# Performance work log

Measured on AMD Instinct MI355X. Metric: run time of the kernel, lower is better.

The kernel has to match this reference:

```python
import jax, jax.numpy as jnp
import numpy as np


def setup_inputs() -> dict:
    key = jax.random.key(0)
    ks = jax.random.split(key, 9)
    N, C, H, W, K = 8, 512, 64, 64, 32
    C4 = C // 4
    s = lambda k, shape, scale=0.02: jax.random.normal(k, shape, dtype=jnp.float32) * scale
    return {
        "x": jax.random.normal(ks[0], (N, C, H, W), dtype=jnp.float32),
        "y": jax.random.normal(ks[1], (N, K, C), dtype=jnp.float32),
        "wq": s(ks[2], (C4, C)),
        "bq": s(ks[3], (C4,)),
        "wk": s(ks[4], (C4, C)),
        "bk": s(ks[5], (C4,)),
        "wv": s(ks[6], (C, C)),
        "bv": s(ks[7], (C,)),
        "scale": s(ks[8], (1,), 1.0),
    }


def reference(x, y, wq, bq, wk, bk, wv, bv, scale):
    N, C, H, W = x.shape
    # 1x1 conv query: (N,C,H,W) -> (N,C4,H,W) -> (N, HW, C4)
    q = jnp.einsum('nchw,oc->nhwo', x, wq) + bq  # (N,H,W,C4)
    q = q.reshape(N, H * W, -1)                   # (N, HW, C4)
    # key/value linears on centers y: (N,K,C)
    k = y @ wk.T + bk                             # (N, K, C4)
    v = y @ wv.T + bv                             # (N, K, C)
    energy = jnp.einsum('npc,nkc->npk', q, k)     # (N, HW, K)
    attn = jax.nn.softmax(energy, axis=-1)
    out = jnp.einsum('nkc,npk->ncp', v, attn)     # (N, C, HW)
    out = out.reshape(N, C, H, W)
    return scale[0] * out + x
```

## Files before the change

### kernel.cpp

```cpp
#include <hip/hip_runtime.h>


#define N_  8
#define C_  512
#define HW_ 4096
#define K_  32

typedef __attribute__((ext_vector_type(8))) short bf16x8;
typedef __attribute__((ext_vector_type(4))) float f32x4;
typedef __attribute__((ext_vector_type(4))) unsigned short u16x4;
typedef __attribute__((ext_vector_type(4))) int i32x4;

__device__ __forceinline__ unsigned short f2b(float f) {
    union { float f; unsigned u; } v; v.f = f;
    unsigned r = v.u + 0x7FFFu + ((v.u >> 16) & 1u);
    return (unsigned short)(r >> 16);
}
__device__ __forceinline__ float b2f(unsigned short h) {
    union { unsigned u; float f; } v; v.u = ((unsigned)h) << 16; return v.f;
}
__device__ __forceinline__ int cvtpk(float a, float b) {
    int r;
    asm("v_cvt_pk_bf16_f32 %0, %1, %2" : "=v"(r) : "v"(a), "v"(b));
    return r;
}

__device__ __forceinline__ int wqk_idx(int kk, int c) {
    return ((((c >> 5) * 2 + (kk >> 4)) * 64 + ((c >> 3) & 3) * 16 + (kk & 15)) << 3) + (c & 7);
}

__global__ __launch_bounds__(256) void prep_kernel(
    const float* __restrict__ y, const float* __restrict__ wq, const float* __restrict__ bq,
    const float* __restrict__ wk, const float* __restrict__ bk,
    const float* __restrict__ wv, const float* __restrict__ bv,
    unsigned short* __restrict__ wqkf, float* __restrict__ bqk, unsigned short* __restrict__ vtf)
{
    const int bid = blockIdx.x;
    const int t = threadIdx.x;

    if (bid < 256) {
        __shared__ float vred[3][4][16][8];
        const int n   = bid >> 5;
        const int ct  = bid & 31;
        const int cl  = t & 15;
        const int kko = (t >> 4) & 3;
        const int jq4 = t >> 6;
        const int c   = ct * 16 + cl;

        const float* yb  = y  + ((size_t)n * K_ + kko * 8) * C_ + jq4 * 128;
        const float* wvb = wv + (size_t)c * C_ + jq4 * 128;
        float acc[8] = {0,0,0,0,0,0,0,0};
        #pragma unroll 4
        for (int jj = 0; jj < 32; ++jj) {
            float4 w4 = *(const float4*)(wvb + jj * 4);
            #pragma unroll
            for (int u = 0; u < 8; ++u) {
                float4 y4 = *(const float4*)(yb + (size_t)u * C_ + jj * 4);
                acc[u] += y4.x * w4.x + y4.y * w4.y + y4.z * w4.z + y4.w * w4.w;
            }
        }
        if (jq4 > 0) {
            #pragma unroll
            for (int u = 0; u < 8; ++u) vred[jq4 - 1][kko][cl][u] = acc[u];
        }
        __syncthreads();
        if (jq4 == 0) {
            const float bvc = bv[c];
            unsigned short o[8];
            #pragma unroll
            for (int u = 0; u < 8; ++u) {
                float s = acc[u] + vred[0][kko][cl][u] + vred[1][kko][cl][u]
                        + vred[2][kko][cl][u] + bvc;
                o[u] = f2b(s);
            }
            i32x4 pk = { (int)(o[0] | ((unsigned)o[1] << 16)), (int)(o[2] | ((unsigned)o[3] << 16)),
                         (int)(o[4] | ((unsigned)o[5] << 16)), (int)(o[6] | ((unsigned)o[7] << 16)) };
            *(i32x4*)(vtf + (size_t)n * (K_ * C_) + (size_t)((ct * 64 + kko * 16 + cl) * 8)) = pk;
        }
    } else {
        __shared__ __align__(16) float kp[2][128];
        __shared__ __align__(16) float kr[128];
        const int b = bid - 256;
        const int n = b >> 5, kk = b & 31;
        const int o = t & 127, half = t >> 7;

        const float* yb  = y  + ((size_t)n * K_ + kk) * C_ + half * 256;
        const float* wkb = wk + (size_t)o * C_ + half * 256;
        float a = 0.f;
        #pragma unroll 4
        for (int jq = 0; jq < 64; ++jq) {
            float4 w4 = *(const float4*)(wkb + jq * 4);
            float4 y4 = *(const float4*)(yb + jq * 4);
            a += y4.x * w4.x + y4.y * w4.y + y4.z * w4.z + y4.w * w4.w;
        }
        kp[half][o] = a;
        __syncthreads();
        if (t < 128) kr[t] = kp[0][t] + kp[1][t] + bk[t];
        __syncthreads();
        if (t < 64) {
            float s = kr[t] * bq[t] + kr[t + 64] * bq[t + 64];
            #pragma unroll
            for (int d = 32; d > 0; d >>= 1) s += __shfl_down(s, d);
            if (t == 0) bqk[n * K_ + kk] = s;
        }
        const int c1 = t, c2 = t + 256;
        float s1 = 0.f, s2 = 0.f;
        for (int oq = 0; oq < 32; ++oq) {
            float4 k4 = *(const float4*)(&kr[oq * 4]);
            const float* wq0 = wq + (size_t)(oq * 4) * C_;
            s1 += k4.x * wq0[c1] + k4.y * wq0[C_ + c1] + k4.z * wq0[2*C_ + c1] + k4.w * wq0[3*C_ + c1];
            s2 += k4.x * wq0[c2] + k4.y * wq0[C_ + c2] + k4.z * wq0[2*C_ + c2] + k4.w * wq0[3*C_ + c2];
        }
        unsigned short* wqf_n = wqkf + (size_t)n * (K_ * C_);
        wqf_n[wqk_idx(kk, c1)] = f2b(s1);
        wqf_n[wqk_idx(kk, c2)] = f2b(s2);
    }
}

__global__ __launch_bounds__(256) void main_kernel(
    const float* __restrict__ x, const unsigned short* __restrict__ wqkf,
    const unsigned short* __restrict__ vtf, const float* __restrict__ bqk,
    const float* __restrict__ scale, float* __restrict__ out)
{
    __shared__ __align__(16) unsigned short xl[16384];
    __shared__ float e_lds[32][36];

    const int bid = (blockIdx.x & 7) * 128 + (blockIdx.x >> 3);
    const int n  = bid >> 7;
    const int p0 = (bid & 127) * 32;
    const int t  = threadIdx.x;
    const int w  = t >> 6, l = t & 63;
    const int l15 = l & 15, lg = l >> 4;
    const float* xg = x + (size_t)n * C_ * HW_;
    float* og = out + (size_t)n * C_ * HW_;
    const unsigned short* wqf  = wqkf + (size_t)n * (K_ * C_);
    const unsigned short* vtfn = vtf  + (size_t)n * (K_ * C_);

    const int mh = w;
    const int kt = w >> 1;
    bf16x8 vf[8];
    #pragma unroll
    for (int mi = 0; mi < 8; ++mi)
        vf[mi] = *(const bf16x8*)(vtfn + ((size_t)(mh * 8 + mi) * 64 + l) * 8);
    bf16x8 b0 = *(const bf16x8*)(wqf + ((size_t)(0 * 2 + kt) * 64 + l) * 8);
    bf16x8 b1 = *(const bf16x8*)(wqf + ((size_t)(1 * 2 + kt) * 64 + l) * 8);

    const int px = t & 31, g = t >> 5;
    const float* xc = xg + p0 + px;
    const int pt = w & 1;
    f32x4 acc = {0.f, 0.f, 0.f, 0.f};
    const unsigned short* xbase = xl + lg * 256 + (pt * 16 + l15) * 8;

    {
        float r0[4][8];
        #pragma unroll
        for (int u = 0; u < 4; ++u)
            #pragma unroll
            for (int j = 0; j < 8; ++j)
                r0[u][j] = xc[(size_t)(g * 8 + u * 64 + j) * HW_];
        #pragma unroll
        for (int u = 0; u < 4; ++u) {
            const int cbase = g * 8 + u * 64;
            const int elem = ((cbase >> 5) * 1024) + (((cbase >> 3) & 3) * 256) + px * 8;
            i32x4 pk = { cvtpk(r0[u][0], r0[u][1]), cvtpk(r0[u][2], r0[u][3]),
                         cvtpk(r0[u][4], r0[u][5]), cvtpk(r0[u][6], r0[u][7]) };
            *(i32x4*)(xl + elem) = pk;
        }
    }
    __syncthreads();

    {
        float r1[4][8];
        #pragma unroll
        for (int u = 0; u < 4; ++u)
            #pragma unroll
            for (int j = 0; j < 8; ++j)
                r1[u][j] = xc[(size_t)(g * 8 + (u + 4) * 64 + j) * HW_];

        for (int cs = 0; cs < 8; ++cs) {
            bf16x8 b2 = *(const bf16x8*)(wqf + ((size_t)((cs + 2) * 2 + kt) * 64 + l) * 8);
            const bf16x8 af = *(const bf16x8*)(xbase + cs * 1024);
            acc = __builtin_amdgcn_mfma_f32_16x16x32_bf16(af, b0, acc, 0, 0, 0);
            b0 = b1; b1 = b2;
        }

        #pragma unroll
        for (int u = 0; u < 4; ++u) {
            const int cbase = g * 8 + (u + 4) * 64;
            const int elem = ((cbase >> 5) * 1024) + (((cbase >> 3) & 3) * 256) + px * 8;
            i32x4 pk = { cvtpk(r1[u][0], r1[u][1]), cvtpk(r1[u][2], r1[u][3]),
                         cvtpk(r1[u][4], r1[u][5]), cvtpk(r1[u][6], r1[u][7]) };
            *(i32x4*)(xl + elem) = pk;
        }
    }
    __syncthreads();

    {
        for (int cs = 8; cs < 16; ++cs) {
            bf16x8 b2;
            if (cs < 14) b2 = *(const bf16x8*)(wqf + ((size_t)((cs + 2) * 2 + kt) * 64 + l) * 8);
            const bf16x8 af = *(const bf16x8*)(xbase + cs * 1024);
            acc = __builtin_amdgcn_mfma_f32_16x16x32_bf16(af, b0, acc, 0, 0, 0);
            b0 = b1; b1 = b2;
        }
        const float bq_ = bqk[n * K_ + kt * 16 + l15];
        #pragma unroll
        for (int r = 0; r < 4; ++r)
            e_lds[pt * 16 + lg * 4 + r][kt * 16 + l15] = acc[r] + bq_;
    }
    __syncthreads();

    bf16x8 paf0, paf1;
    {
        float e0[32], e1[32];
        #pragma unroll
        for (int i = 0; i < 8; ++i) {
            float4 q0 = *(const float4*)&e_lds[l15][4 * i];
            float4 q1 = *(const float4*)&e_lds[16 + l15][4 * i];
            e0[4*i] = q0.x; e0[4*i+1] = q0.y; e0[4*i+2] = q0.z; e0[4*i+3] = q0.w;
            e1[4*i] = q1.x; e1[4*i+1] = q1.y; e1[4*i+2] = q1.z; e1[4*i+3] = q1.w;
        }
        float m0 = e0[0], m1 = e1[0];
        #pragma unroll
        for (int k = 1; k < 32; ++k) { m0 = fmaxf(m0, e0[k]); m1 = fmaxf(m1, e1[k]); }
        float s0 = 0.f, s1 = 0.f;
        #pragma unroll
        for (int k = 0; k < 32; ++k) {
            e0[k] = __expf(e0[k] - m0); s0 += e0[k];
            e1[k] = __expf(e1[k] - m1); s1 += e1[k];
        }
        const float i0 = 1.f / s0, i1 = 1.f / s1;
        union { int i[4]; bf16x8 v; } u0, u1;
        #pragma unroll
        for (int jj = 0; jj < 4; ++jj) {
            u0.i[jj] = cvtpk(e0[8*lg + 2*jj] * i0, e0[8*lg + 2*jj + 1] * i0);
            u1.i[jj] = cvtpk(e1[8*lg + 2*jj] * i1, e1[8*lg + 2*jj + 1] * i1);
        }
        paf0 = u0.v; paf1 = u1.v;
    }

    {
        const float fs = scale[0];
        const int pxa = p0 + l15, pxb = p0 + 16 + l15;
        const int mt0 = mh * 8;

        #pragma unroll
        for (int mi = 0; mi < 8; ++mi) {
            const int mt = mt0 + mi;
            f32x4 d0 = __builtin_amdgcn_mfma_f32_16x16x32_bf16(vf[mi], paf0, (f32x4){0.f,0.f,0.f,0.f}, 0, 0, 0);
            f32x4 d1 = __builtin_amdgcn_mfma_f32_16x16x32_bf16(vf[mi], paf1, (f32x4){0.f,0.f,0.f,0.f}, 0, 0, 0);
            const int base = (mt >> 1) * 1024 + ((2 * mt + (lg >> 1)) & 3) * 256 + (lg & 1) * 4;
            const u16x4 ra = *(const u16x4*)(xl + base + l15 * 8);
            const u16x4 rb = *(const u16x4*)(xl + base + (16 + l15) * 8);
            const int cc = mt * 16 + lg * 4;
            #pragma unroll
            for (int r = 0; r < 4; ++r) {
                og[(size_t)(cc + r) * HW_ + pxa] = fs * d0[r] + b2f(ra[r]);
                og[(size_t)(cc + r) * HW_ + pxb] = fs * d1[r] + b2f(rb[r]);
            }
        }
    }
}

extern "C" void kernel_launch(void* const* d_in, const int* in_sizes, int n_in,
                              void* d_out, int out_size, void* d_ws, size_t ws_size,
                              hipStream_t stream) {
    const float* x     = (const float*)d_in[0];
    const float* y     = (const float*)d_in[1];
    const float* wq    = (const float*)d_in[2];
    const float* bq    = (const float*)d_in[3];
    const float* wk    = (const float*)d_in[4];
    const float* bk    = (const float*)d_in[5];
    const float* wv    = (const float*)d_in[6];
    const float* bv    = (const float*)d_in[7];
    const float* scale = (const float*)d_in[8];

    unsigned short* wqkf = (unsigned short*)d_ws;
    unsigned short* vtf  = wqkf + (size_t)N_ * K_ * C_;
    float* bqk = (float*)((char*)d_ws + 524288);

    prep_kernel<<<512, 256, 0, stream>>>(y, wq, bq, wk, bk, wv, bv, wqkf, bqk, vtf);
    main_kernel<<<1024, 256, 0, stream>>>(x, wqkf, vtf, bqk, scale, (float*)d_out);
}
```

Measured before the change: 54.70 us.

## Process two pixel tiles per block with double-buffered LDS prefetch

Each block now handles two consecutive 32-pixel tiles, and the grid is halved to 512 blocks. The x slab for the second tile is loaded from global memory into registers and written into a second LDS buffer while the first tile's energy, softmax and output stages run. The V fragments, bias and scale are loaded once and reused for both tiles. The cost is double the LDS footprint (64KB for x), which reduces occupancy, and fewer blocks in flight. Overlap within a block also shrinks, because the first tile's x load is no longer split around the first half of the QK MFMAs.

```diff
diff --git a/kernel.cpp b/kernel.cpp
--- a/kernel.cpp
+++ b/kernel.cpp
@@ -122,12 +122,12 @@
     const unsigned short* __restrict__ vtf, const float* __restrict__ bqk,
     const float* __restrict__ scale, float* __restrict__ out)
 {
-    __shared__ __align__(16) unsigned short xl[16384];
+    __shared__ __align__(16) unsigned short xl[2][16384];
     __shared__ float e_lds[32][36];
 
-    const int bid = (blockIdx.x & 7) * 128 + (blockIdx.x >> 3);
-    const int n  = bid >> 7;
-    const int p0 = (bid & 127) * 32;
+    const int swz = (blockIdx.x & 7) * 64 + (blockIdx.x >> 3);
+    const int n    = swz >> 6;
+    const int pair = swz & 63;
     const int t  = threadIdx.x;
     const int w  = t >> 6, l = t & 63;
     const int l15 = l & 15, lg = l >> 4;
@@ -138,127 +138,147 @@
 
     const int mh = w;
     const int kt = w >> 1;
+    const int pt = w & 1;
+    const int px = t & 31, g = t >> 5;
+    const float fs = scale[0];
+    const float bq_ = bqk[n * K_ + kt * 16 + l15];
+
     bf16x8 vf[8];
     #pragma unroll
     for (int mi = 0; mi < 8; ++mi)
         vf[mi] = *(const bf16x8*)(vtfn + ((size_t)(mh * 8 + mi) * 64 + l) * 8);
-    bf16x8 b0 = *(const bf16x8*)(wqf + ((size_t)(0 * 2 + kt) * 64 + l) * 8);
-    bf16x8 b1 = *(const bf16x8*)(wqf + ((size_t)(1 * 2 + kt) * 64 + l) * 8);
-
-    const int px = t & 31, g = t >> 5;
-    const float* xc = xg + p0 + px;
-    const int pt = w & 1;
-    f32x4 acc = {0.f, 0.f, 0.f, 0.f};
-    const unsigned short* xbase = xl + lg * 256 + (pt * 16 + l15) * 8;
 
     {
-        float r0[4][8];
+        const float* xc = xg + pair * 64 + px;
+        float r[4][8];
         #pragma unroll
-        for (int u = 0; u < 4; ++u)
-            #pragma unroll
-            for (int j = 0; j < 8; ++j)
-                r0[u][j] = xc[(size_t)(g * 8 + u * 64 + j) * HW_];
-        #pragma unroll
-        for (int u = 0; u < 4; ++u) {
-            const int cbase = g * 8 + u * 64;
-            const int elem = ((cbase >> 5) * 1024) + (((cbase >> 3) & 3) * 256) + px * 8;
-            i32x4 pk = { cvtpk(r0[u][0], r0[u][1]), cvtpk(r0[u][2], r0[u][3]),
-                         cvtpk(r0[u][4], r0[u][5]), cvtpk(r0[u][6], r0[u][7]) };
-            *(i32x4*)(xl + elem) = pk;
+        for (int h = 0; h < 2; ++h) {
+            #pragma unroll
+            for (int u = 0; u < 4; ++u)
+                #pragma unroll
+                for (int j = 0; j < 8; ++j)
+                    r[u][j] = xc[(size_t)(g * 8 + (h * 4 + u) * 64 + j) * HW_];
+            #pragma unroll
+            for (int u = 0; u < 4; ++u) {
+                const int cbase = g * 8 + (h * 4 + u) * 64;
+                const int elem = ((cbase >> 5) * 1024) + (((cbase >> 3) & 3) * 256) + px * 8;
+                i32x4 pk = { cvtpk(r[u][0], r[u][1]), cvtpk(r[u][2], r[u][3]),
+                             cvtpk(r[u][4], r[u][5]), cvtpk(r[u][6], r[u][7]) };
+                *(i32x4*)(&xl[0][elem]) = pk;
+            }
         }
     }
     __syncthreads();
 
-    {
-        float r1[4][8];
-        #pragma unroll
-        for (int u = 0; u < 4; ++u)
-            #pragma unroll
-            for (int j = 0; j < 8; ++j)
-                r1[u][j] = xc[(size_t)(g * 8 + (u + 4) * 64 + j) * HW_];
-
-        for (int cs = 0; cs < 8; ++cs) {
-            bf16x8 b2 = *(const bf16x8*)(wqf + ((size_t)((cs + 2) * 2 + kt) * 64 + l) * 8);
-            const bf16x8 af = *(const bf16x8*)(xbase + cs * 1024);
-            acc = __builtin_amdgcn_mfma_f32_16x16x32_bf16(af, b0, acc, 0, 0, 0);
-            b0 = b1; b1 = b2;
-        }
-
-        #pragma unroll
-        for (int u = 0; u < 4; ++u) {
-            const int cbase = g * 8 + (u + 4) * 64;
-            const int elem = ((cbase >> 5) * 1024) + (((cbase >> 3) & 3) * 256) + px * 8;
-            i32x4 pk = { cvtpk(r1[u][0], r1[u][1]), cvtpk(r1[u][2], r1[u][3]),
-                         cvtpk(r1[u][4], r1[u][5]), cvtpk(r1[u][6], r1[u][7]) };
-            *(i32x4*)(xl + elem) = pk;
-        }
-    }
-    __syncthreads();
-
-    {
-        for (int cs = 8; cs < 16; ++cs) {
-            bf16x8 b2;
-            if (cs < 14) b2 = *(const bf16x8*)(wqf + ((size_t)((cs + 2) * 2 + kt) * 64 + l) * 8);
-            const bf16x8 af = *(const bf16x8*)(xbase + cs * 1024);
-            acc = __builtin_amdgcn_mfma_f32_16x16x32_bf16(af, b0, acc, 0, 0, 0);
-            b0 = b1; b1 = b2;
-        }
-        const float bq_ = bqk[n * K_ + kt * 16 + l15];
-        #pragma unroll
-        for (int r = 0; r < 4; ++r)
-            e_lds[pt * 16 + lg * 4 + r][kt * 16 + l15] = acc[r] + bq_;
-    }
-    __syncthreads();
-
-    bf16x8 paf0, paf1;
-    {
-        float e0[32], e1[32];
-        #pragma unroll
-        for (int i = 0; i < 8; ++i) {
-            float4 q0 = *(const float4*)&e_lds[l15][4 * i];
-            float4 q1 = *(const float4*)&e_lds[16 + l15][4 * i];
-            e0[4*i] = q0.x; e0[4*i+1] = q0.y; e0[4*i+2] = q0.z; e0[4*i+3] = q0.w;
-            e1[4*i] = q1.x; e1[4*i+1] = q1.y; e1[4*i+2] = q1.z; e1[4*i+3] = q1.w;
-        }
-        float m0 = e0[0], m1 = e1[0];
-        #pragma unroll
-        for (int k = 1; k < 32; ++k) { m0 = fmaxf(m0, e0[k]); m1 = fmaxf(m1, e1[k]); }
-        float s0 = 0.f, s1 = 0.f;
-        #pragma unroll
-        for (int k = 0; k < 32; ++k) {
-            e0[k] = __expf(e0[k] - m0); s0 += e0[k];
-            e1[k] = __expf(e1[k] - m1); s1 += e1[k];
-        }
-        const float i0 = 1.f / s0, i1 = 1.f / s1;
-        union { int i[4]; bf16x8 v; } u0, u1;
-        #pragma unroll
-        for (int jj = 0; jj < 4; ++jj) {
-            u0.i[jj] = cvtpk(e0[8*lg + 2*jj] * i0, e0[8*lg + 2*jj + 1] * i0);
-            u1.i[jj] = cvtpk(e1[8*lg + 2*jj] * i1, e1[8*lg + 2*jj + 1] * i1);
-        }
-        paf0 = u0.v; paf1 = u1.v;
-    }
-
-    {
-        const float fs = scale[0];
-        const int pxa = p0 + l15, pxb = p0 + 16 + l15;
-        const int mt0 = mh * 8;
-
-        #pragma unroll
-        for (int mi = 0; mi < 8; ++mi) {
-            const int mt = mt0 + mi;
-            f32x4 d0 = __builtin_amdgcn_mfma_f32_16x16x32_bf16(vf[mi], paf0, (f32x4){0.f,0.f,0.f,0.f}, 0, 0, 0);
-            f32x4 d1 = __builtin_amdgcn_mfma_f32_16x16x32_bf16(vf[mi], paf1, (f32x4){0.f,0.f,0.f,0.f}, 0, 0, 0);
-            const int base = (mt >> 1) * 1024 + ((2 * mt + (lg >> 1)) & 3) * 256 + (lg & 1) * 4;
-            const u16x4 ra = *(const u16x4*)(xl + base + l15 * 8);
-            const u16x4 rb = *(const u16x4*)(xl + base + (16 + l15) * 8);
-            const int cc = mt * 16 + lg * 4;
-            #pragma unroll
-            for (int r = 0; r < 4; ++r) {
-                og[(size_t)(cc + r) * HW_ + pxa] = fs * d0[r] + b2f(ra[r]);
-                og[(size_t)(cc + r) * HW_ + pxb] = fs * d1[r] + b2f(rb[r]);
-            }
-        }
+    for (int i = 0; i < 2; ++i) {
+        const unsigned short* xb = xl[i];
+        unsigned short* xw = xl[1 - i];
+        const float* xcn = xg + pair * 64 + 32 + px;
+        float rs[4][8];
+
+        if (i == 0) {
+            #pragma unroll
+            for (int u = 0; u < 4; ++u)
+                #pragma unroll
+                for (int j = 0; j < 8; ++j)
+                    rs[u][j] = xcn[(size_t)(g * 8 + u * 64 + j) * HW_];
+        }
+
+        {
+            bf16x8 b0 = *(const bf16x8*)(wqf + ((size_t)(0 * 2 + kt) * 64 + l) * 8);
+            bf16x8 b1 = *(const bf16x8*)(wqf + ((size_t)(1 * 2 + kt) * 64 + l) * 8);
+            f32x4 acc = {0.f, 0.f, 0.f, 0.f};
+            const unsigned short* xbase = xb + lg * 256 + (pt * 16 + l15) * 8;
+            for (int cs = 0; cs < 16; ++cs) {
+                bf16x8 b2;
+                if (cs < 14) b2 = *(const bf16x8*)(wqf + ((size_t)((cs + 2) * 2 + kt) * 64 + l) * 8);
+                const bf16x8 af = *(const bf16x8*)(xbase + cs * 1024);
+                acc = __builtin_amdgcn_mfma_f32_16x16x32_bf16(af, b0, acc, 0, 0, 0);
+                b0 = b1; b1 = b2;
+            }
+            #pragma unroll
+            for (int r = 0; r < 4; ++r)
+                e_lds[pt * 16 + lg * 4 + r][kt * 16 + l15] = acc[r] + bq_;
+        }
+
+        if (i == 0) {
+            #pragma unroll
+            for (int u = 0; u < 4; ++u) {
+                const int cbase = g * 8 + u * 64;
+                const int elem = ((cbase >> 5) * 1024) + (((cbase >> 3) & 3) * 256) + px * 8;
+                i32x4 pk = { cvtpk(rs[u][0], rs[u][1]), cvtpk(rs[u][2], rs[u][3]),
+                             cvtpk(rs[u][4], rs[u][5]), cvtpk(rs[u][6], rs[u][7]) };
+                *(i32x4*)(&xw[elem]) = pk;
+            }
+            #pragma unroll
+            for (int u = 0; u < 4; ++u)
+                #pragma unroll
+                for (int j = 0; j < 8; ++j)
+                    rs[u][j] = xcn[(size_t)(g * 8 + (u + 4) * 64 + j) * HW_];
+        }
+        __syncthreads();
+
+        bf16x8 paf0, paf1;
+        {
+            float e0[32], e1[32];
+            #pragma unroll
+            for (int q = 0; q < 8; ++q) {
+                float4 q0 = *(const float4*)&e_lds[l15][4 * q];
+                float4 q1 = *(const float4*)&e_lds[16 + l15][4 * q];
+                e0[4*q] = q0.x; e0[4*q+1] = q0.y; e0[4*q+2] = q0.z; e0[4*q+3] = q0.w;
+                e1[4*q] = q1.x; e1[4*q+1] = q1.y; e1[4*q+2] = q1.z; e1[4*q+3] = q1.w;
+            }
+            float m0 = e0[0], m1 = e1[0];
+            #pragma unroll
+            for (int k = 1; k < 32; ++k) { m0 = fmaxf(m0, e0[k]); m1 = fmaxf(m1, e1[k]); }
+            float s0 = 0.f, s1 = 0.f;
+            #pragma unroll
+            for (int k = 0; k < 32; ++k) {
+                e0[k] = __expf(e0[k] - m0); s0 += e0[k];
+                e1[k] = __expf(e1[k] - m1); s1 += e1[k];
+            }
+            const float i0 = 1.f / s0, i1 = 1.f / s1;
+            union { int q[4]; bf16x8 v; } u0, u1;
+            #pragma unroll
+            for (int jj = 0; jj < 4; ++jj) {
+                u0.q[jj] = cvtpk(e0[8*lg + 2*jj] * i0, e0[8*lg + 2*jj + 1] * i0);
+                u1.q[jj] = cvtpk(e1[8*lg + 2*jj] * i1, e1[8*lg + 2*jj + 1] * i1);
+            }
+            paf0 = u0.v; paf1 = u1.v;
+        }
+
+        {
+            const int p0i = pair * 64 + i * 32;
+            const int pxa = p0i + l15, pxb = p0i + 16 + l15;
+            const int mt0 = mh * 8;
+            #pragma unroll
+            for (int mi = 0; mi < 8; ++mi) {
+                const int mt = mt0 + mi;
+                f32x4 d0 = __builtin_amdgcn_mfma_f32_16x16x32_bf16(vf[mi], paf0, (f32x4){0.f,0.f,0.f,0.f}, 0, 0, 0);
+                f32x4 d1 = __builtin_amdgcn_mfma_f32_16x16x32_bf16(vf[mi], paf1, (f32x4){0.f,0.f,0.f,0.f}, 0, 0, 0);
+                const int base = (mt >> 1) * 1024 + ((2 * mt + (lg >> 1)) & 3) * 256 + (lg & 1) * 4;
+                const u16x4 ra = *(const u16x4*)(xb + base + l15 * 8);
+                const u16x4 rb = *(const u16x4*)(xb + base + (16 + l15) * 8);
+                const int cc = mt * 16 + lg * 4;
+                #pragma unroll
+                for (int r = 0; r < 4; ++r) {
+                    og[(size_t)(cc + r) * HW_ + pxa] = fs * d0[r] + b2f(ra[r]);
+                    og[(size_t)(cc + r) * HW_ + pxb] = fs * d1[r] + b2f(rb[r]);
+                }
+            }
+        }
+
+        if (i == 0) {
+            #pragma unroll
+            for (int u = 0; u < 4; ++u) {
+                const int cbase = g * 8 + (u + 4) * 64;
+                const int elem = ((cbase >> 5) * 1024) + (((cbase >> 3) & 3) * 256) + px * 8;
+                i32x4 pk = { cvtpk(rs[u][0], rs[u][1]), cvtpk(rs[u][2], rs[u][3]),
+                             cvtpk(rs[u][4], rs[u][5]), cvtpk(rs[u][6], rs[u][7]) };
+                *(i32x4*)(&xw[elem]) = pk;
+            }
+        }
+        __syncthreads();
     }
 }
 
@@ -280,5 +300,5 @@
     float* bqk = (float*)((char*)d_ws + 524288);
 
     prep_kernel<<<512, 256, 0, stream>>>(y, wq, bq, wk, bk, wv, bv, wqkf, bqk, vtf);
-    main_kernel<<<1024, 256, 0, stream>>>(x, wqkf, vtf, bqk, scale, (float*)d_out);
-}
+    main_kernel<<<512, 256, 0, stream>>>(x, wqkf, vtf, bqk, scale, (float*)d_out);
+}
```

New measurement: 64.32 us. +17.6%, slower.

## Halve x LDS buffer and reread fp32 residual from global memory

Applied to the files above, without the earlier changes.

The x tile in LDS shrinks from 16384 to 8192 bf16 entries. The second half of the channels now overwrites the first half after an added barrier, so the buffer is reused as a ring. The residual add no longer reads the bf16-rounded x from LDS. It reloads fp32 x from global memory with a one-step software prefetch, which also gives the exact fp32 residual. The smaller LDS footprint could allow more resident blocks, but the kernel now reads x from global twice and adds a synchronization.

```diff
diff --git a/kernel.cpp b/kernel.cpp
--- a/kernel.cpp
+++ b/kernel.cpp
@@ -8,16 +8,12 @@
 
 typedef __attribute__((ext_vector_type(8))) short bf16x8;
 typedef __attribute__((ext_vector_type(4))) float f32x4;
-typedef __attribute__((ext_vector_type(4))) unsigned short u16x4;
 typedef __attribute__((ext_vector_type(4))) int i32x4;
 
 __device__ __forceinline__ unsigned short f2b(float f) {
     union { float f; unsigned u; } v; v.f = f;
     unsigned r = v.u + 0x7FFFu + ((v.u >> 16) & 1u);
     return (unsigned short)(r >> 16);
-}
-__device__ __forceinline__ float b2f(unsigned short h) {
-    union { unsigned u; float f; } v; v.u = ((unsigned)h) << 16; return v.f;
 }
 __device__ __forceinline__ int cvtpk(float a, float b) {
     int r;
@@ -122,7 +118,7 @@
     const unsigned short* __restrict__ vtf, const float* __restrict__ bqk,
     const float* __restrict__ scale, float* __restrict__ out)
 {
-    __shared__ __align__(16) unsigned short xl[16384];
+    __shared__ __align__(16) unsigned short xl[8192];
     __shared__ float e_lds[32][36];
 
     const int bid = (blockIdx.x & 7) * 128 + (blockIdx.x >> 3);
@@ -161,7 +157,7 @@
         #pragma unroll
         for (int u = 0; u < 4; ++u) {
             const int cbase = g * 8 + u * 64;
-            const int elem = ((cbase >> 5) * 1024) + (((cbase >> 3) & 3) * 256) + px * 8;
+            const int elem = (((cbase >> 5) & 7) * 1024) + (((cbase >> 3) & 3) * 256) + px * 8;
             i32x4 pk = { cvtpk(r0[u][0], r0[u][1]), cvtpk(r0[u][2], r0[u][3]),
                          cvtpk(r0[u][4], r0[u][5]), cvtpk(r0[u][6], r0[u][7]) };
             *(i32x4*)(xl + elem) = pk;
@@ -169,8 +165,8 @@
     }
     __syncthreads();
 
-    {
-        float r1[4][8];
+    float r1[4][8];
+    {
         #pragma unroll
         for (int u = 0; u < 4; ++u)
             #pragma unroll
@@ -183,11 +179,14 @@
             acc = __builtin_amdgcn_mfma_f32_16x16x32_bf16(af, b0, acc, 0, 0, 0);
             b0 = b1; b1 = b2;
         }
-
+    }
+    __syncthreads();
+
+    {
         #pragma unroll
         for (int u = 0; u < 4; ++u) {
             const int cbase = g * 8 + (u + 4) * 64;
-            const int elem = ((cbase >> 5) * 1024) + (((cbase >> 3) & 3) * 256) + px * 8;
+            const int elem = (((cbase >> 5) & 7) * 1024) + (((cbase >> 3) & 3) * 256) + px * 8;
             i32x4 pk = { cvtpk(r1[u][0], r1[u][1]), cvtpk(r1[u][2], r1[u][3]),
                          cvtpk(r1[u][4], r1[u][5]), cvtpk(r1[u][6], r1[u][7]) };
             *(i32x4*)(xl + elem) = pk;
@@ -199,7 +198,7 @@
         for (int cs = 8; cs < 16; ++cs) {
             bf16x8 b2;
             if (cs < 14) b2 = *(const bf16x8*)(wqf + ((size_t)((cs + 2) * 2 + kt) * 64 + l) * 8);
-            const bf16x8 af = *(const bf16x8*)(xbase + cs * 1024);
+            const bf16x8 af = *(const bf16x8*)(xbase + (cs & 7) * 1024);
             acc = __builtin_amdgcn_mfma_f32_16x16x32_bf16(af, b0, acc, 0, 0, 0);
             b0 = b1; b1 = b2;
         }
@@ -244,20 +243,36 @@
         const int pxa = p0 + l15, pxb = p0 + 16 + l15;
         const int mt0 = mh * 8;
 
-        #pragma unroll
+        float xr0[4], xr1[4];
+        {
+            const int c0 = mt0 * 16 + lg * 4;
+            #pragma unroll
+            for (int r = 0; r < 4; ++r) {
+                xr0[r] = xg[(size_t)(c0 + r) * HW_ + pxa];
+                xr1[r] = xg[(size_t)(c0 + r) * HW_ + pxb];
+            }
+        }
         for (int mi = 0; mi < 8; ++mi) {
             const int mt = mt0 + mi;
+            float y0[4], y1[4];
+            if (mi < 7) {
+                const int cn = (mt + 1) * 16 + lg * 4;
+                #pragma unroll
+                for (int r = 0; r < 4; ++r) {
+                    y0[r] = xg[(size_t)(cn + r) * HW_ + pxa];
+                    y1[r] = xg[(size_t)(cn + r) * HW_ + pxb];
+                }
+            }
             f32x4 d0 = __builtin_amdgcn_mfma_f32_16x16x32_bf16(vf[mi], paf0, (f32x4){0.f,0.f,0.f,0.f}, 0, 0, 0);
             f32x4 d1 = __builtin_amdgcn_mfma_f32_16x16x32_bf16(vf[mi], paf1, (f32x4){0.f,0.f,0.f,0.f}, 0, 0, 0);
-            const int base = (mt >> 1) * 1024 + ((2 * mt + (lg >> 1)) & 3) * 256 + (lg & 1) * 4;
-            const u16x4 ra = *(const u16x4*)(xl + base + l15 * 8);
-            const u16x4 rb = *(const u16x4*)(xl + base + (16 + l15) * 8);
             const int cc = mt * 16 + lg * 4;
             #pragma unroll
             for (int r = 0; r < 4; ++r) {
-                og[(size_t)(cc + r) * HW_ + pxa] = fs * d0[r] + b2f(ra[r]);
-                og[(size_t)(cc + r) * HW_ + pxb] = fs * d1[r] + b2f(rb[r]);
-            }
+                og[(size_t)(cc + r) * HW_ + pxa] = fs * d0[r] + xr0[r];
+                og[(size_t)(cc + r) * HW_ + pxb] = fs * d1[r] + xr1[r];
+            }
+            #pragma unroll
+            for (int r = 0; r < 4; ++r) { xr0[r] = y0[r]; xr1[r] = y1[r]; }
         }
     }
 }
```

Measured after the change: 66.15 us. 20.9% more time.
